# Optimization experiments

Hardware: AMD Instinct MI355X
Metric: run time of the kernel (lower is better)

The kernel has to match this reference:

```python
import jax, jax.numpy as jnp
import numpy as np

N_NODES = 100000
N_EDGES = 1600000
IN_FEATS = 128
HIDDEN = 128
N_CLASSES = 40
EPS = 1e-5  # BatchNorm1d default eps


def setup_inputs():
    key = jax.random.key(0)
    ks = jax.random.split(key, 12)
    s_in = 1.0 / np.sqrt(IN_FEATS)
    s_h = 1.0 / np.sqrt(HIDDEN)
    return {
        "feat": jax.random.normal(ks[0], (N_NODES, IN_FEATS), jnp.float32),
        "src": jax.random.randint(ks[1], (N_EDGES,), 0, N_NODES, jnp.int32),
        "dst": jax.random.randint(ks[2], (N_EDGES,), 0, N_NODES, jnp.int32),
        # GraphConv weights, stored (out, in) as in the torch module
        "w0": jax.random.normal(ks[3], (HIDDEN, IN_FEATS), jnp.float32) * s_in,
        "w1": jax.random.normal(ks[4], (HIDDEN, HIDDEN), jnp.float32) * s_h,
        "w2": jax.random.normal(ks[5], (N_CLASSES, HIDDEN), jnp.float32) * s_h,
        "b2": jnp.zeros((N_CLASSES,), jnp.float32),  # bias only on last layer
        # skip-connection linears (use_linear=True, bias=False)
        "l0": jax.random.normal(ks[6], (HIDDEN, IN_FEATS), jnp.float32) * s_in,
        "l1": jax.random.normal(ks[7], (HIDDEN, HIDDEN), jnp.float32) * s_h,
        "l2": jax.random.normal(ks[8], (N_CLASSES, HIDDEN), jnp.float32) * s_h,
        # BatchNorm affine params for the two hidden layers
        "g0": jnp.ones((HIDDEN,), jnp.float32),
        "beta0": jnp.zeros((HIDDEN,), jnp.float32),
        "g1": jnp.ones((HIDDEN,), jnp.float32),
        "beta1": jnp.zeros((HIDDEN,), jnp.float32),
    }


def _spmm(h, src, dst):
    # copy_u + sum aggregation: out[d] = sum_{e: dst[e]==d} h[src[e]]
    return jax.ops.segment_sum(h[src], dst, num_segments=N_NODES)


def gcn_forward(feat, src, dst, w0, w1, w2, b2, l0, l1, l2, g0, beta0, g1, beta1):
    ones = jnp.ones((src.shape[0],), jnp.float32)
    out_deg = jnp.clip(jax.ops.segment_sum(ones, src, num_segments=N_NODES), 1.0)
    in_deg = jnp.clip(jax.ops.segment_sum(ones, dst, num_segments=N_NODES), 1.0)
    out_norm = out_deg ** -0.5  # norm='both', applied to src features
    in_norm = in_deg ** -0.5    # norm='both', applied to aggregated result

    def conv(h, W, bias, in_gt_out):
        hs = h * out_norm[:, None]
        if in_gt_out:  # in_feats > out_feats: project first, then aggregate
            rst = _spmm(hs @ W.T, src, dst)
        else:          # aggregate first, then project
            rst = _spmm(hs, src, dst) @ W.T
        rst = rst * in_norm[:, None]
        if bias is not None:
            rst = rst + bias
        return rst

    def bn(x, g, b):
        mu = x.mean(0)
        var = x.var(0)  # biased variance, matches BN training-mode normalization
        return (x - mu) * jax.lax.rsqrt(var + EPS) * g + b

    h = feat  # dropout in eval mode = identity
    h = jax.nn.relu(bn(conv(h, w0, None, IN_FEATS > HIDDEN) + h @ l0.T, g0, beta0))
    h = jax.nn.relu(bn(conv(h, w1, None, False) + h @ l1.T, g1, beta1))
    h = conv(h, w2, b2, HIDDEN > N_CLASSES) + h @ l2.T
    return h


def reference(feat, src, dst, w0, w1, w2, b2, l0, l1, l2, g0, beta0, g1, beta1):
    return gcn_forward(feat, src, dst, w0, w1, w2, b2, l0, l1, l2, g0, beta0, g1, beta1)
```

## Files before the change

### kernel.cpp

```cpp
#include <hip/hip_runtime.h>
#include <hip/hip_fp16.h>
#include <cstdint>
#include <cstddef>

#define N_NODES 100000
#define N_EDGES 1600000
#define EPS 1e-5f

typedef _Float16 half8 __attribute__((ext_vector_type(8)));
typedef float floatx4 __attribute__((ext_vector_type(4)));

#define HCH 128
#define HRG 4
#define HBINS 32768
#define HWORDS (HBINS / 2)
#define HCHUNK (N_EDGES / HCH)
#define HCHUNK4 (HCHUNK / 4)

__global__ void k_hist_part(const int* __restrict__ keys, unsigned int* __restrict__ Hpart) {
  __shared__ unsigned int bins[HWORDS];
  int c = blockIdx.x % HCH, r = blockIdx.x / HCH;
  int base = r * HBINS;
  for (int i = threadIdx.x; i < HWORDS; i += 256) bins[i] = 0;
  __syncthreads();
  const int4* k4 = (const int4*)(keys + c * HCHUNK);
  for (int i = threadIdx.x; i < HCHUNK4; i += 256) {
    int4 k = k4[i];
    int a;
    a = k.x - base; if ((unsigned)a < (unsigned)HBINS) atomicAdd(&bins[a >> 1], 1u << ((a & 1) * 16));
    a = k.y - base; if ((unsigned)a < (unsigned)HBINS) atomicAdd(&bins[a >> 1], 1u << ((a & 1) * 16));
    a = k.z - base; if ((unsigned)a < (unsigned)HBINS) atomicAdd(&bins[a >> 1], 1u << ((a & 1) * 16));
    a = k.w - base; if ((unsigned)a < (unsigned)HBINS) atomicAdd(&bins[a >> 1], 1u << ((a & 1) * 16));
  }
  __syncthreads();
  unsigned int* outp = Hpart + ((size_t)blockIdx.x << 14);
  for (int i = threadIdx.x; i < HWORDS; i += 256) outp[i] = bins[i];
}

__global__ void k_hist_sum(const unsigned short* __restrict__ Hp, int* __restrict__ deg) {
  int b = blockIdx.x * 256 + threadIdx.x;
  if (b >= N_NODES) return;
  int r = b >> 15, lo = b & (HBINS - 1);
  const unsigned short* p = Hp + ((size_t)(r * HCH) << 15) + lo;
  unsigned int t = 0;
#pragma unroll 8
  for (int c = 0; c < HCH; ++c) t += p[(size_t)c << 15];
  deg[b] = (int)t;
}

__global__ void k_hist_scan(unsigned short* __restrict__ Hp, int* __restrict__ degd) {
  int b = blockIdx.x * 256 + threadIdx.x;
  if (b >= N_NODES) return;
  int r = b >> 15, lo = b & (HBINS - 1);
  unsigned short* p = Hp + ((size_t)(r * HCH) << 15) + lo;
  unsigned int t = 0;
#pragma unroll 8
  for (int c = 0; c < HCH; ++c) {
    unsigned int v = p[(size_t)c << 15];
    p[(size_t)c << 15] = (unsigned short)t;
    t += v;
  }
  degd[b] = (int)t;
}

__global__ void k_build(const int* __restrict__ src, const int* __restrict__ dst,
                        const unsigned short* __restrict__ Hbase,
                        const int* __restrict__ row_start, int* __restrict__ col) {
  __shared__ unsigned int cur[HWORDS];
  int c = blockIdx.x % HCH, r = blockIdx.x / HCH;
  int base = r * HBINS;
  for (int i = threadIdx.x; i < HWORDS; i += 256) cur[i] = 0;
  __syncthreads();
  const unsigned short* hb = Hbase + ((size_t)blockIdx.x << 15);
  const int4* d4 = (const int4*)(dst + c * HCHUNK);
  const int4* s4 = (const int4*)(src + c * HCHUNK);
  for (int i = threadIdx.x; i < HCHUNK4; i += 256) {
    int4 d = d4[i];
    int4 s = s4[i];
    int a;
    a = d.x - base;
    if ((unsigned)a < (unsigned)HBINS) {
      unsigned old = atomicAdd(&cur[a >> 1], 1u << ((a & 1) * 16));
      unsigned lr = (old >> ((a & 1) * 16)) & 0xffffu;
      col[row_start[d.x] + hb[a] + lr] = s.x;
    }
    a = d.y - base;
    if ((unsigned)a < (unsigned)HBINS) {
      unsigned old = atomicAdd(&cur[a >> 1], 1u << ((a & 1) * 16));
      unsigned lr = (old >> ((a & 1) * 16)) & 0xffffu;
      col[row_start[d.y] + hb[a] + lr] = s.y;
    }
    a = d.z - base;
    if ((unsigned)a < (unsigned)HBINS) {
      unsigned old = atomicAdd(&cur[a >> 1], 1u << ((a & 1) * 16));
      unsigned lr = (old >> ((a & 1) * 16)) & 0xffffu;
      col[row_start[d.z] + hb[a] + lr] = s.z;
    }
    a = d.w - base;
    if ((unsigned)a < (unsigned)HBINS) {
      unsigned old = atomicAdd(&cur[a >> 1], 1u << ((a & 1) * 16));
      unsigned lr = (old >> ((a & 1) * 16)) & 0xffffu;
      col[row_start[d.w] + hb[a] + lr] = s.w;
    }
  }
}

__global__ void k_norms(const int* __restrict__ degs, const int* __restrict__ degd,
                        float* out_norm, float* in_norm) {
  int i = blockIdx.x * 256 + threadIdx.x;
  if (i < N_NODES) {
    out_norm[i] = rsqrtf((float)max(degs[i], 1));
    in_norm[i]  = rsqrtf((float)max(degd[i], 1));
  }
}

__global__ void k_scan1(const int* __restrict__ degd, int* bsum) {
  __shared__ int s[256];
  int t = threadIdx.x;
  int i = blockIdx.x * 256 + t;
  s[t] = (i < N_NODES) ? degd[i] : 0;
  __syncthreads();
  for (int off = 128; off > 0; off >>= 1) {
    if (t < off) s[t] += s[t + off];
    __syncthreads();
  }
  if (t == 0) bsum[blockIdx.x] = s[0];
}

__global__ void k_scan2(int* bsum, int nb) {
  __shared__ int s[512];
  int t = threadIdx.x;
  int v = (t < nb) ? bsum[t] : 0;
  s[t] = v;
  __syncthreads();
  for (int off = 1; off < 512; off <<= 1) {
    int x = (t >= off) ? s[t - off] : 0;
    __syncthreads();
    s[t] += x;
    __syncthreads();
  }
  if (t < nb) bsum[t] = s[t] - v;
}

__global__ void k_scan3(const int* __restrict__ degd, const int* __restrict__ bsum,
                        int* row_start) {
  __shared__ int s[256];
  int t = threadIdx.x;
  int i = blockIdx.x * 256 + t;
  int v = (i < N_NODES) ? degd[i] : 0;
  s[t] = v;
  __syncthreads();
  for (int off = 1; off < 256; off <<= 1) {
    int x = (t >= off) ? s[t - off] : 0;
    __syncthreads();
    s[t] += x;
    __syncthreads();
  }
  if (i < N_NODES) row_start[i] = bsum[blockIdx.x] + s[t] - v;
  if (i == 0) row_start[N_NODES] = N_EDGES;
}

__global__ void k_w2h(const float* __restrict__ w0, const float* __restrict__ l0,
                      const float* __restrict__ w1, const float* __restrict__ l1,
                      const float* __restrict__ w2, const float* __restrict__ l2,
                      unsigned short* __restrict__ W) {
  int i = blockIdx.x * 256 + threadIdx.x;
  if (i >= 18944) return;
  int h = i * 4;
  const float* src; int off;
  if (h < 16384)      { src = w0; off = h; }
  else if (h < 32768) { src = l0; off = h - 16384; }
  else if (h < 49152) { src = w1; off = h - 32768; }
  else if (h < 65536) { src = l1; off = h - 49152; }
  else if (h < 70656) { src = w2; off = h - 65536; }
  else                { src = l2; off = h - 70656; }
  float4 v = *(const float4*)(src + off);
  ushort4 o;
  o.x = __half_as_ushort(__float2half_rn(v.x));
  o.y = __half_as_ushort(__float2half_rn(v.y));
  o.z = __half_as_ushort(__float2half_rn(v.z));
  o.w = __half_as_ushort(__float2half_rn(v.w));
  ((ushort4*)W)[i] = o;
}

__global__ void k_feat2h(const float* __restrict__ feat, const float* __restrict__ out_norm,
                         unsigned short* __restrict__ H, unsigned short* __restrict__ F) {
  int i = blockIdx.x * 256 + threadIdx.x;
  if (i >= N_NODES * 32) return;
  float on = out_norm[i >> 5];
  float4 v = ((const float4*)feat)[i];
  ushort4 s, u;
  s.x = __half_as_ushort(__float2half_rn(v.x * on));
  s.y = __half_as_ushort(__float2half_rn(v.y * on));
  s.z = __half_as_ushort(__float2half_rn(v.z * on));
  s.w = __half_as_ushort(__float2half_rn(v.w * on));
  u.x = __half_as_ushort(__float2half_rn(v.x));
  u.y = __half_as_ushort(__float2half_rn(v.y));
  u.z = __half_as_ushort(__float2half_rn(v.z));
  u.w = __half_as_ushort(__float2half_rn(v.w));
  ((ushort4*)H)[i] = s;
  ((ushort4*)F)[i] = u;
}

__global__ void k_agg128h(const __half* __restrict__ H, const int* __restrict__ col,
                          const int* __restrict__ row_start,
                          const float* __restrict__ in_norm,
                          unsigned short* __restrict__ out16) {
  int wave = threadIdx.x >> 6;
  int lane = threadIdx.x & 63;
  int node = blockIdx.x * 4 + wave;
  if (node >= N_NODES) return;
  int q = lane >> 4;
  int sub = lane & 15;
  int s0 = row_start[node], s1 = row_start[node + 1];
  const uint4* hp = (const uint4*)H;
  float a[8];
#pragma unroll
  for (int j = 0; j < 8; ++j) a[j] = 0.f;
  int e = s0 + q;
  for (; e + 4 < s1; e += 8) {
    int c0 = col[e];
    int c1 = col[e + 4];
    uint4 u0 = hp[(size_t)c0 * 16 + sub];
    uint4 u1 = hp[(size_t)c1 * 16 + sub];
    const __half2* h0 = (const __half2*)&u0;
    const __half2* h1 = (const __half2*)&u1;
#pragma unroll
    for (int j = 0; j < 4; ++j) {
      float2 f0 = __half22float2(h0[j]);
      float2 f1 = __half22float2(h1[j]);
      a[2 * j] += f0.x + f1.x;
      a[2 * j + 1] += f0.y + f1.y;
    }
  }
  if (e < s1) {
    uint4 u = hp[(size_t)col[e] * 16 + sub];
    const __half2* h0 = (const __half2*)&u;
#pragma unroll
    for (int j = 0; j < 4; ++j) {
      float2 f = __half22float2(h0[j]);
      a[2 * j] += f.x;
      a[2 * j + 1] += f.y;
    }
  }
#pragma unroll
  for (int j = 0; j < 8; ++j) {
    a[j] += __shfl_xor(a[j], 16);
    a[j] += __shfl_xor(a[j], 32);
  }
  if (q == 0) {
    float sc = in_norm[node];
    __half2 o[4];
#pragma unroll
    for (int j = 0; j < 4; ++j)
      o[j] = __float22half2_rn(make_float2(a[2 * j] * sc, a[2 * j + 1] * sc));
    ((uint4*)out16)[(size_t)node * 16 + sub] = *(const uint4*)o;
  }
}

__launch_bounds__(256)
__global__ void k_gemm_dual16(const unsigned short* __restrict__ Xa,
                              const unsigned short* __restrict__ Xh,
                              const unsigned short* __restrict__ W16,
                              unsigned short* __restrict__ Out16, float* __restrict__ pstats) {
  __shared__ __align__(16) unsigned short sX[64][136];
  __shared__ __align__(16) unsigned short sW[128][136];
  int t = threadIdx.x;
  int row0 = blockIdx.x * 64;
  int w = t >> 6, lane = t & 63;
  int q = lane >> 4, m = lane & 15;
  floatx4 acc[8];
#pragma unroll
  for (int i = 0; i < 8; ++i) acc[i] = (floatx4){0.f, 0.f, 0.f, 0.f};

  for (int phase = 0; phase < 2; ++phase) {
    const unsigned short* Xg = phase ? Xh : Xa;
    __syncthreads();
    {
#pragma unroll
      for (int it = 0; it < 4; ++it) {
        int idx = it * 256 + t;
        int r = idx >> 4, g = idx & 15;
        const uint4* xr = (const uint4*)(Xg + (size_t)min(row0 + r, N_NODES - 1) * 128);
        *(uint4*)&sX[r][g * 8] = xr[g];
      }
    }
    {
      const uint4* wsrc = (const uint4*)(W16 + ((size_t)phase << 14));
#pragma unroll
      for (int it = 0; it < 8; ++it) {
        int idx = it * 256 + t;
        int n = idx >> 4, g = idx & 15;
        *(uint4*)&sW[n][g * 8] = wsrc[idx];
      }
    }
    __syncthreads();
#pragma unroll
    for (int ks = 0; ks < 4; ++ks) {
      int kk = ks * 32 + q * 8;
      half8 a = *(const half8*)&sX[w * 16 + m][kk];
#pragma unroll
      for (int t8 = 0; t8 < 8; ++t8) {
        half8 b = *(const half8*)&sW[t8 * 16 + m][kk];
        acc[t8] = __builtin_amdgcn_mfma_f32_16x16x32_f16(a, b, acc[t8], 0, 0, 0);
      }
    }
  }
  float ps[8], pq[8];
#pragma unroll
  for (int t8 = 0; t8 < 8; ++t8) {
    int colj = t8 * 16 + m;
    float s = 0.f, sq = 0.f;
#pragma unroll
    for (int i = 0; i < 4; ++i) {
      int row = row0 + w * 16 + q * 4 + i;
      if (row < N_NODES) {
        float v = acc[t8][i];
        s += v; sq += v * v;
        Out16[(size_t)row * 128 + colj] = __half_as_ushort(__float2half_rn(v));
      }
    }
    s += __shfl_xor(s, 16);
    s += __shfl_xor(s, 32);
    sq += __shfl_xor(sq, 16);
    sq += __shfl_xor(sq, 32);
    ps[t8] = s; pq[t8] = sq;
  }
  __syncthreads();
  float* pSum = (float*)&sX[0][0];
  float* pSq = pSum + 512;
  if (q == 0) {
#pragma unroll
    for (int t8 = 0; t8 < 8; ++t8) {
      pSum[w * 128 + t8 * 16 + m] = ps[t8];
      pSq[w * 128 + t8 * 16 + m] = pq[t8];
    }
  }
  __syncthreads();
  if (t < 128) {
    float s = (pSum[t] + pSum[128 + t]) + (pSum[256 + t] + pSum[384 + t]);
    float sq = (pSq[t] + pSq[128 + t]) + (pSq[256 + t] + pSq[384 + t]);
    pstats[(size_t)blockIdx.x * 256 + t] = s;
    pstats[(size_t)blockIdx.x * 256 + 128 + t] = sq;
  }
}

__global__ void k_stats_red(const float* __restrict__ pstats, float* __restrict__ stats,
                            int nblk) {
  int t = threadIdx.x;
  float s = 0.f;
  for (int b = blockIdx.x; b < nblk; b += gridDim.x)
    s += pstats[(size_t)b * 256 + t];
  atomicAdd(&stats[t], s);
}

__global__ void k_bnrelu16(const unsigned short* __restrict__ x16,
                           const float* __restrict__ stats,
                           const float* __restrict__ g, const float* __restrict__ b,
                           const float* __restrict__ out_norm,
                           unsigned short* __restrict__ H, unsigned short* __restrict__ F) {
  int i = blockIdx.x * 256 + threadIdx.x;
  if (i >= N_NODES * 16) return;
  int c8 = (i & 15) * 8;
  uint4 raw = ((const uint4*)x16)[i];
  const __half2* hp2 = (const __half2*)&raw;
  float v[8];
#pragma unroll
  for (int j = 0; j < 4; ++j) {
    float2 f = __half22float2(hp2[j]);
    v[2 * j] = f.x;
    v[2 * j + 1] = f.y;
  }
  const float inv = 1.f / (float)N_NODES;
#pragma unroll
  for (int j = 0; j < 8; ++j) {
    int c = c8 + j;
    float mu = stats[c] * inv;
    float var = stats[128 + c] * inv - mu * mu;
    float rs = rsqrtf(var + EPS);
    float y = (v[j] - mu) * rs * g[c] + b[c];
    v[j] = y > 0.f ? y : 0.f;
  }
  if (H) {
    float on = out_norm[i >> 4];
    ushort4 o[2];
#pragma unroll
    for (int j = 0; j < 8; ++j) ((unsigned short*)o)[j] = __half_as_ushort(__float2half_rn(v[j] * on));
    ((uint4*)H)[i] = *(const uint4*)o;
  }
  if (F) {
    ushort4 o[2];
#pragma unroll
    for (int j = 0; j < 8; ++j) ((unsigned short*)o)[j] = __half_as_ushort(__float2half_rn(v[j]));
    ((uint4*)F)[i] = *(const uint4*)o;
  }
}

__launch_bounds__(256)
__global__ void k_gemm2_16(const unsigned short* __restrict__ X,
                           const unsigned short* __restrict__ W80,
                           const float* __restrict__ b2,
                           const float* __restrict__ out_norm,
                           __half* __restrict__ p, float* __restrict__ out) {
  __shared__ __align__(16) unsigned short sX[64][136];
  __shared__ __align__(16) unsigned short sW[80][136];
  int t = threadIdx.x;
  int row0 = blockIdx.x * 64;
  int w = t >> 6, lane = t & 63;
  int q = lane >> 4, m = lane & 15;
  {
#pragma unroll
    for (int it = 0; it < 4; ++it) {
      int idx = it * 256 + t;
      int r = idx >> 4, g = idx & 15;
      const uint4* xr = (const uint4*)(X + (size_t)min(row0 + r, N_NODES - 1) * 128);
      *(uint4*)&sX[r][g * 8] = xr[g];
    }
  }
  {
    const uint4* wsrc = (const uint4*)W80;
#pragma unroll
    for (int it = 0; it < 5; ++it) {
      int idx = it * 256 + t;
      int n = idx >> 4, g = idx & 15;
      *(uint4*)&sW[n][g * 8] = wsrc[idx];
    }
  }
  __syncthreads();
  floatx4 acc[5];
#pragma unroll
  for (int i = 0; i < 5; ++i) acc[i] = (floatx4){0.f, 0.f, 0.f, 0.f};
#pragma unroll
  for (int ks = 0; ks < 4; ++ks) {
    int kk = ks * 32 + q * 8;
    half8 a = *(const half8*)&sX[w * 16 + m][kk];
#pragma unroll
    for (int t5 = 0; t5 < 5; ++t5) {
      half8 b = *(const half8*)&sW[t5 * 16 + m][kk];
      acc[t5] = __builtin_amdgcn_mfma_f32_16x16x32_f16(a, b, acc[t5], 0, 0, 0);
    }
  }
#pragma unroll
  for (int t5 = 0; t5 < 5; ++t5) {
    int col = t5 * 16 + m;
#pragma unroll
    for (int i = 0; i < 4; ++i) {
      int row = row0 + w * 16 + q * 4 + i;
      if (row >= N_NODES) continue;
      if (col < 40) {
        p[(size_t)row * 64 + col] = __float2half_rn(out_norm[row] * acc[t5][i]);
      } else {
        out[(size_t)row * 40 + (col - 40)] = acc[t5][i] + b2[col - 40];
      }
    }
  }
  for (int idx = t; idx < 64 * 24; idx += 256) {
    int r = idx / 24, c = 40 + idx % 24;
    int row = row0 + r;
    if (row < N_NODES) p[(size_t)row * 64 + c] = __float2half_rn(0.f);
  }
}

__global__ void k_agg64h(const __half* __restrict__ p, const int* __restrict__ col,
                         const int* __restrict__ row_start,
                         const float* __restrict__ in_norm,
                         float* __restrict__ out) {
  int wave = threadIdx.x >> 6, lane = threadIdx.x & 63;
  int node = blockIdx.x * 4 + wave;
  if (node >= N_NODES) return;
  int oct = lane >> 3;
  int sub = lane & 7;
  int s0 = row_start[node], s1 = row_start[node + 1];
  const uint4* pp = (const uint4*)p;
  float a[8];
#pragma unroll
  for (int j = 0; j < 8; ++j) a[j] = 0.f;
  int e = s0 + oct;
  for (; e + 8 < s1; e += 16) {
    int c0 = col[e];
    int c1 = col[e + 8];
    uint4 u0 = pp[(size_t)c0 * 8 + sub];
    uint4 u1 = pp[(size_t)c1 * 8 + sub];
    const __half2* h0 = (const __half2*)&u0;
    const __half2* h1 = (const __half2*)&u1;
#pragma unroll
    for (int j = 0; j < 4; ++j) {
      float2 f0 = __half22float2(h0[j]);
      float2 f1 = __half22float2(h1[j]);
      a[2 * j] += f0.x + f1.x;
      a[2 * j + 1] += f0.y + f1.y;
    }
  }
  if (e < s1) {
    uint4 u = pp[(size_t)col[e] * 8 + sub];
    const __half2* h0 = (const __half2*)&u;
#pragma unroll
    for (int j = 0; j < 4; ++j) {
      float2 f = __half22float2(h0[j]);
      a[2 * j] += f.x;
      a[2 * j + 1] += f.y;
    }
  }
#pragma unroll
  for (int j = 0; j < 8; ++j) {
    a[j] += __shfl_xor(a[j], 8);
    a[j] += __shfl_xor(a[j], 16);
    a[j] += __shfl_xor(a[j], 32);
  }
  if (oct == 0 && sub < 5) {
    float sc = in_norm[node];
    float4* op = (float4*)(out + (size_t)node * 40 + (size_t)sub * 8);
    float4 v0 = op[0], v1 = op[1];
    v0.x += sc * a[0]; v0.y += sc * a[1]; v0.z += sc * a[2]; v0.w += sc * a[3];
    v1.x += sc * a[4]; v1.y += sc * a[5]; v1.z += sc * a[6]; v1.w += sc * a[7];
    op[0] = v0; op[1] = v1;
  }
}

extern "C" void kernel_launch(void* const* d_in, const int* in_sizes, int n_in,
                              void* d_out, int out_size, void* d_ws, size_t ws_size,
                              hipStream_t stream) {
  const float* feat = (const float*)d_in[0];
  const int* src = (const int*)d_in[1];
  const int* dst = (const int*)d_in[2];
  const float* w0 = (const float*)d_in[3];
  const float* w1 = (const float*)d_in[4];
  const float* w2 = (const float*)d_in[5];
  const float* b2 = (const float*)d_in[6];
  const float* l0 = (const float*)d_in[7];
  const float* l1 = (const float*)d_in[8];
  const float* l2 = (const float*)d_in[9];
  const float* g0 = (const float*)d_in[10];
  const float* beta0 = (const float*)d_in[11];
  const float* g1 = (const float*)d_in[12];
  const float* beta1 = (const float*)d_in[13];
  float* out = (float*)d_out;

  char* ws = (char*)d_ws;
  size_t off = 0;
  auto alloc = [&](size_t bytes) {
    void* ptr = ws + off;
    off = (off + bytes + 255) & ~(size_t)255;
    return ptr;
  };
  unsigned short* A16 = (unsigned short*)alloc(2 * (size_t)N_NODES * 128);
  float* B = (float*)alloc(sizeof(float) * (size_t)N_NODES * 128);
  unsigned short* H = (unsigned short*)alloc(2 * (size_t)N_NODES * 128);
  unsigned short* F = (unsigned short*)alloc(2 * (size_t)N_NODES * 128);
  int* degs = (int*)alloc(sizeof(int) * N_NODES);
  int* degd = (int*)alloc(sizeof(int) * N_NODES);
  int* row_start = (int*)alloc(sizeof(int) * (N_NODES + 1));
  int* colb = (int*)alloc(sizeof(int) * N_EDGES);
  float* out_norm = (float*)alloc(sizeof(float) * N_NODES);
  float* in_norm = (float*)alloc(sizeof(float) * N_NODES);
  int* bsum = (int*)alloc(sizeof(int) * 512);
  float* stats = (float*)alloc(sizeof(float) * 256);
  unsigned short* W16 = (unsigned short*)alloc(2 * (size_t)75776);
  int gb = (N_NODES + 63) / 64;
  float* pstats = (float*)alloc(sizeof(float) * (size_t)gb * 256);

  unsigned int* Hpart = (unsigned int*)B;
  unsigned short* B16 = (unsigned short*)B;

  int nb = (N_NODES + 255) / 256;
  int hb = HCH * HRG;

  k_w2h<<<74, 256, 0, stream>>>(w0, l0, w1, l1, w2, l2, W16);

  k_hist_part<<<hb, 256, 0, stream>>>(src, Hpart);
  k_hist_sum<<<nb, 256, 0, stream>>>((const unsigned short*)Hpart, degs);
  k_hist_part<<<hb, 256, 0, stream>>>(dst, Hpart);
  k_hist_scan<<<nb, 256, 0, stream>>>((unsigned short*)Hpart, degd);
  k_norms<<<nb, 256, 0, stream>>>(degs, degd, out_norm, in_norm);
  k_scan1<<<nb, 256, 0, stream>>>(degd, bsum);
  k_scan2<<<1, 512, 0, stream>>>(bsum, nb);
  k_scan3<<<nb, 256, 0, stream>>>(degd, bsum, row_start);
  k_build<<<hb, 256, 0, stream>>>(src, dst, (const unsigned short*)Hpart, row_start, colb);

  int ab = (N_NODES + 3) / 4;
  int fb = (N_NODES * 32 + 255) / 256;
  int hb16 = (N_NODES * 16 + 255) / 256;

  k_feat2h<<<fb, 256, 0, stream>>>(feat, out_norm, H, F);
  k_agg128h<<<ab, 256, 0, stream>>>((const __half*)H, colb, row_start, in_norm, A16);
  k_gemm_dual16<<<gb, 256, 0, stream>>>(A16, F, W16, B16, pstats);
  hipMemsetAsync(stats, 0, sizeof(float) * 256, stream);
  k_stats_red<<<32, 256, 0, stream>>>(pstats, stats, gb);
  k_bnrelu16<<<hb16, 256, 0, stream>>>(B16, stats, g0, beta0, out_norm, H, F);

  k_agg128h<<<ab, 256, 0, stream>>>((const __half*)H, colb, row_start, in_norm, A16);
  k_gemm_dual16<<<gb, 256, 0, stream>>>(A16, F, W16 + 32768, B16, pstats);
  hipMemsetAsync(stats, 0, sizeof(float) * 256, stream);
  k_stats_red<<<32, 256, 0, stream>>>(pstats, stats, gb);
  k_bnrelu16<<<hb16, 256, 0, stream>>>(B16, stats, g1, beta1, out_norm,
                                       (unsigned short*)nullptr, F);

  __half* p = (__half*)A16;
  k_gemm2_16<<<gb, 256, 0, stream>>>(F, W16 + 65536, b2, out_norm, p, out);
  k_agg64h<<<ab, 256, 0, stream>>>(p, colb, row_start, in_norm, out);
}
```

Measured before the change: 509.8 us.

## Replace histogram CSR build with global atomics and chunk-split aggregation

Swaps the partitioned shared-memory histogram and prefix-offset CSR build for direct global atomic degree counting and atomic cursor-based column placement. Splits 128-wide aggregation into 8 feature chunks, each handled by its own blocks and written in a chunk-major layout, so the gather of each chunk can stay cache-resident. The GEMM load is updated to read that chunked layout. Global atomics may contend, make the in-row edge order nondeterministic, and the chunked aggregation reissues the column-index reads for every chunk.

```diff
diff --git a/kernel.cpp b/kernel.cpp
--- a/kernel.cpp
+++ b/kernel.cpp
@@ -10,99 +10,16 @@
 typedef _Float16 half8 __attribute__((ext_vector_type(8)));
 typedef float floatx4 __attribute__((ext_vector_type(4)));
 
-#define HCH 128
-#define HRG 4
-#define HBINS 32768
-#define HWORDS (HBINS / 2)
-#define HCHUNK (N_EDGES / HCH)
-#define HCHUNK4 (HCHUNK / 4)
-
-__global__ void k_hist_part(const int* __restrict__ keys, unsigned int* __restrict__ Hpart) {
-  __shared__ unsigned int bins[HWORDS];
-  int c = blockIdx.x % HCH, r = blockIdx.x / HCH;
-  int base = r * HBINS;
-  for (int i = threadIdx.x; i < HWORDS; i += 256) bins[i] = 0;
-  __syncthreads();
-  const int4* k4 = (const int4*)(keys + c * HCHUNK);
-  for (int i = threadIdx.x; i < HCHUNK4; i += 256) {
-    int4 k = k4[i];
-    int a;
-    a = k.x - base; if ((unsigned)a < (unsigned)HBINS) atomicAdd(&bins[a >> 1], 1u << ((a & 1) * 16));
-    a = k.y - base; if ((unsigned)a < (unsigned)HBINS) atomicAdd(&bins[a >> 1], 1u << ((a & 1) * 16));
-    a = k.z - base; if ((unsigned)a < (unsigned)HBINS) atomicAdd(&bins[a >> 1], 1u << ((a & 1) * 16));
-    a = k.w - base; if ((unsigned)a < (unsigned)HBINS) atomicAdd(&bins[a >> 1], 1u << ((a & 1) * 16));
-  }
-  __syncthreads();
-  unsigned int* outp = Hpart + ((size_t)blockIdx.x << 14);
-  for (int i = threadIdx.x; i < HWORDS; i += 256) outp[i] = bins[i];
-}
-
-__global__ void k_hist_sum(const unsigned short* __restrict__ Hp, int* __restrict__ deg) {
-  int b = blockIdx.x * 256 + threadIdx.x;
-  if (b >= N_NODES) return;
-  int r = b >> 15, lo = b & (HBINS - 1);
-  const unsigned short* p = Hp + ((size_t)(r * HCH) << 15) + lo;
-  unsigned int t = 0;
-#pragma unroll 8
-  for (int c = 0; c < HCH; ++c) t += p[(size_t)c << 15];
-  deg[b] = (int)t;
-}
-
-__global__ void k_hist_scan(unsigned short* __restrict__ Hp, int* __restrict__ degd) {
-  int b = blockIdx.x * 256 + threadIdx.x;
-  if (b >= N_NODES) return;
-  int r = b >> 15, lo = b & (HBINS - 1);
-  unsigned short* p = Hp + ((size_t)(r * HCH) << 15) + lo;
-  unsigned int t = 0;
-#pragma unroll 8
-  for (int c = 0; c < HCH; ++c) {
-    unsigned int v = p[(size_t)c << 15];
-    p[(size_t)c << 15] = (unsigned short)t;
-    t += v;
-  }
-  degd[b] = (int)t;
-}
-
-__global__ void k_build(const int* __restrict__ src, const int* __restrict__ dst,
-                        const unsigned short* __restrict__ Hbase,
-                        const int* __restrict__ row_start, int* __restrict__ col) {
-  __shared__ unsigned int cur[HWORDS];
-  int c = blockIdx.x % HCH, r = blockIdx.x / HCH;
-  int base = r * HBINS;
-  for (int i = threadIdx.x; i < HWORDS; i += 256) cur[i] = 0;
-  __syncthreads();
-  const unsigned short* hb = Hbase + ((size_t)blockIdx.x << 15);
-  const int4* d4 = (const int4*)(dst + c * HCHUNK);
-  const int4* s4 = (const int4*)(src + c * HCHUNK);
-  for (int i = threadIdx.x; i < HCHUNK4; i += 256) {
-    int4 d = d4[i];
-    int4 s = s4[i];
-    int a;
-    a = d.x - base;
-    if ((unsigned)a < (unsigned)HBINS) {
-      unsigned old = atomicAdd(&cur[a >> 1], 1u << ((a & 1) * 16));
-      unsigned lr = (old >> ((a & 1) * 16)) & 0xffffu;
-      col[row_start[d.x] + hb[a] + lr] = s.x;
-    }
-    a = d.y - base;
-    if ((unsigned)a < (unsigned)HBINS) {
-      unsigned old = atomicAdd(&cur[a >> 1], 1u << ((a & 1) * 16));
-      unsigned lr = (old >> ((a & 1) * 16)) & 0xffffu;
-      col[row_start[d.y] + hb[a] + lr] = s.y;
-    }
-    a = d.z - base;
-    if ((unsigned)a < (unsigned)HBINS) {
-      unsigned old = atomicAdd(&cur[a >> 1], 1u << ((a & 1) * 16));
-      unsigned lr = (old >> ((a & 1) * 16)) & 0xffffu;
-      col[row_start[d.z] + hb[a] + lr] = s.z;
-    }
-    a = d.w - base;
-    if ((unsigned)a < (unsigned)HBINS) {
-      unsigned old = atomicAdd(&cur[a >> 1], 1u << ((a & 1) * 16));
-      unsigned lr = (old >> ((a & 1) * 16)) & 0xffffu;
-      col[row_start[d.w] + hb[a] + lr] = s.w;
-    }
-  }
+__global__ void k_deg(const int* __restrict__ src, const int* __restrict__ dst,
+                      int* __restrict__ degs, int* __restrict__ degd) {
+  int i = blockIdx.x * 256 + threadIdx.x;
+  if (i >= N_EDGES / 4) return;
+  int4 s = ((const int4*)src)[i];
+  int4 d = ((const int4*)dst)[i];
+  atomicAdd(&degs[s.x], 1); atomicAdd(&degs[s.y], 1);
+  atomicAdd(&degs[s.z], 1); atomicAdd(&degs[s.w], 1);
+  atomicAdd(&degd[d.x], 1); atomicAdd(&degd[d.y], 1);
+  atomicAdd(&degd[d.z], 1); atomicAdd(&degd[d.w], 1);
 }
 
 __global__ void k_norms(const int* __restrict__ degs, const int* __restrict__ degd,
@@ -158,6 +75,24 @@
   }
   if (i < N_NODES) row_start[i] = bsum[blockIdx.x] + s[t] - v;
   if (i == 0) row_start[N_NODES] = N_EDGES;
+}
+
+__global__ void k_initcur(const int* __restrict__ row_start, int* __restrict__ cur) {
+  int i = blockIdx.x * 256 + threadIdx.x;
+  if (i < N_NODES) cur[i] = row_start[i];
+}
+
+__global__ void k_build2(const int* __restrict__ src, const int* __restrict__ dst,
+                         int* __restrict__ cur, int* __restrict__ col) {
+  int i = blockIdx.x * 256 + threadIdx.x;
+  if (i >= N_EDGES / 4) return;
+  int4 s = ((const int4*)src)[i];
+  int4 d = ((const int4*)dst)[i];
+  int p;
+  p = atomicAdd(&cur[d.x], 1); col[p] = s.x;
+  p = atomicAdd(&cur[d.y], 1); col[p] = s.y;
+  p = atomicAdd(&cur[d.z], 1); col[p] = s.z;
+  p = atomicAdd(&cur[d.w], 1); col[p] = s.w;
 }
 
 __global__ void k_w2h(const float* __restrict__ w0, const float* __restrict__ l0,
@@ -202,59 +137,49 @@
   ((ushort4*)F)[i] = u;
 }
 
-__global__ void k_agg128h(const __half* __restrict__ H, const int* __restrict__ col,
-                          const int* __restrict__ row_start,
-                          const float* __restrict__ in_norm,
-                          unsigned short* __restrict__ out16) {
-  int wave = threadIdx.x >> 6;
-  int lane = threadIdx.x & 63;
-  int node = blockIdx.x * 4 + wave;
-  if (node >= N_NODES) return;
-  int q = lane >> 4;
-  int sub = lane & 15;
-  int s0 = row_start[node], s1 = row_start[node + 1];
+__global__ void k_aggc(const unsigned short* __restrict__ H, const int* __restrict__ col,
+                       const int* __restrict__ row_start, const float* __restrict__ in_norm,
+                       unsigned short* __restrict__ out16c) {
+  int chunk = blockIdx.x & 7;
+  int grp = blockIdx.x >> 3;
+  int t = threadIdx.x;
+  int lane = t & 63;
+  int wv = t >> 6;
+  int node = grp * 128 + wv * 32 + (lane >> 1);
+  int sub = lane & 1;
+  bool valid = node < N_NODES;
+  int s0 = 0, s1 = 0;
+  if (valid) { s0 = row_start[node]; s1 = row_start[node + 1]; }
   const uint4* hp = (const uint4*)H;
+  size_t coff = (size_t)chunk * 2 + sub;
   float a[8];
 #pragma unroll
   for (int j = 0; j < 8; ++j) a[j] = 0.f;
-  int e = s0 + q;
-  for (; e + 4 < s1; e += 8) {
-    int c0 = col[e];
-    int c1 = col[e + 4];
-    uint4 u0 = hp[(size_t)c0 * 16 + sub];
-    uint4 u1 = hp[(size_t)c1 * 16 + sub];
-    const __half2* h0 = (const __half2*)&u0;
-    const __half2* h1 = (const __half2*)&u1;
-#pragma unroll
-    for (int j = 0; j < 4; ++j) {
-      float2 f0 = __half22float2(h0[j]);
-      float2 f1 = __half22float2(h1[j]);
-      a[2 * j] += f0.x + f1.x;
-      a[2 * j + 1] += f0.y + f1.y;
-    }
-  }
-  if (e < s1) {
-    uint4 u = hp[(size_t)col[e] * 16 + sub];
-    const __half2* h0 = (const __half2*)&u;
-#pragma unroll
-    for (int j = 0; j < 4; ++j) {
-      float2 f = __half22float2(h0[j]);
-      a[2 * j] += f.x;
-      a[2 * j + 1] += f.y;
-    }
-  }
-#pragma unroll
-  for (int j = 0; j < 8; ++j) {
-    a[j] += __shfl_xor(a[j], 16);
-    a[j] += __shfl_xor(a[j], 32);
-  }
-  if (q == 0) {
+  int e = s0;
+  while (__any(e < s1)) {
+#pragma unroll
+    for (int k = 0; k < 4; ++k) {
+      if (e + k < s1) {
+        int c = col[e + k];
+        uint4 u = hp[(size_t)c * 16 + coff];
+        const __half2* h2p = (const __half2*)&u;
+#pragma unroll
+        for (int j = 0; j < 4; ++j) {
+          float2 f = __half22float2(h2p[j]);
+          a[2 * j] += f.x;
+          a[2 * j + 1] += f.y;
+        }
+      }
+    }
+    e += 4;
+  }
+  if (valid) {
     float sc = in_norm[node];
     __half2 o[4];
 #pragma unroll
     for (int j = 0; j < 4; ++j)
       o[j] = __float22half2_rn(make_float2(a[2 * j] * sc, a[2 * j + 1] * sc));
-    ((uint4*)out16)[(size_t)node * 16 + sub] = *(const uint4*)o;
+    ((uint4*)out16c)[((size_t)chunk * N_NODES + node) * 2 + sub] = *(const uint4*)o;
   }
 }
 
@@ -274,14 +199,24 @@
   for (int i = 0; i < 8; ++i) acc[i] = (floatx4){0.f, 0.f, 0.f, 0.f};
 
   for (int phase = 0; phase < 2; ++phase) {
-    const unsigned short* Xg = phase ? Xh : Xa;
-    __syncthreads();
-    {
+    __syncthreads();
+    if (phase == 0) {
+      const uint4* xc = (const uint4*)Xa;
+#pragma unroll
+      for (int it = 0; it < 4; ++it) {
+        int idx = it * 256 + t;
+        int p = idx >> 7;
+        int n = (idx >> 1) & 63;
+        int sb = idx & 1;
+        int row = min(row0 + n, N_NODES - 1);
+        *(uint4*)&sX[n][p * 16 + sb * 8] = xc[((size_t)p * N_NODES + row) * 2 + sb];
+      }
+    } else {
 #pragma unroll
       for (int it = 0; it < 4; ++it) {
         int idx = it * 256 + t;
         int r = idx >> 4, g = idx & 15;
-        const uint4* xr = (const uint4*)(Xg + (size_t)min(row0 + r, N_NODES - 1) * 128);
+        const uint4* xr = (const uint4*)(Xh + (size_t)min(row0 + r, N_NODES - 1) * 128);
         *(uint4*)&sX[r][g * 8] = xr[g];
       }
     }
@@ -558,37 +493,38 @@
   unsigned short* W16 = (unsigned short*)alloc(2 * (size_t)75776);
   int gb = (N_NODES + 63) / 64;
   float* pstats = (float*)alloc(sizeof(float) * (size_t)gb * 256);
-
-  unsigned int* Hpart = (unsigned int*)B;
+  int* cursor = (int*)alloc(sizeof(int) * N_NODES);
+
   unsigned short* B16 = (unsigned short*)B;
 
   int nb = (N_NODES + 255) / 256;
-  int hb = HCH * HRG;
+  int eb4 = (N_EDGES / 4 + 255) / 256;
 
   k_w2h<<<74, 256, 0, stream>>>(w0, l0, w1, l1, w2, l2, W16);
 
-  k_hist_part<<<hb, 256, 0, stream>>>(src, Hpart);
-  k_hist_sum<<<nb, 256, 0, stream>>>((const unsigned short*)Hpart, degs);
-  k_hist_part<<<hb, 256, 0, stream>>>(dst, Hpart);
-  k_hist_scan<<<nb, 256, 0, stream>>>((unsigned short*)Hpart, degd);
+  hipMemsetAsync(degs, 0, sizeof(int) * N_NODES, stream);
+  hipMemsetAsync(degd, 0, sizeof(int) * N_NODES, stream);
+  k_deg<<<eb4, 256, 0, stream>>>(src, dst, degs, degd);
   k_norms<<<nb, 256, 0, stream>>>(degs, degd, out_norm, in_norm);
   k_scan1<<<nb, 256, 0, stream>>>(degd, bsum);
   k_scan2<<<1, 512, 0, stream>>>(bsum, nb);
   k_scan3<<<nb, 256, 0, stream>>>(degd, bsum, row_start);
-  k_build<<<hb, 256, 0, stream>>>(src, dst, (const unsigned short*)Hpart, row_start, colb);
+  k_initcur<<<nb, 256, 0, stream>>>(row_start, cursor);
+  k_build2<<<eb4, 256, 0, stream>>>(src, dst, cursor, colb);
 
   int ab = (N_NODES + 3) / 4;
+  int cb = 8 * ((N_NODES + 127) / 128);
   int fb = (N_NODES * 32 + 255) / 256;
   int hb16 = (N_NODES * 16 + 255) / 256;
 
   k_feat2h<<<fb, 256, 0, stream>>>(feat, out_norm, H, F);
-  k_agg128h<<<ab, 256, 0, stream>>>((const __half*)H, colb, row_start, in_norm, A16);
+  k_aggc<<<cb, 256, 0, stream>>>(H, colb, row_start, in_norm, A16);
   k_gemm_dual16<<<gb, 256, 0, stream>>>(A16, F, W16, B16, pstats);
   hipMemsetAsync(stats, 0, sizeof(float) * 256, stream);
   k_stats_red<<<32, 256, 0, stream>>>(pstats, stats, gb);
   k_bnrelu16<<<hb16, 256, 0, stream>>>(B16, stats, g0, beta0, out_norm, H, F);
 
-  k_agg128h<<<ab, 256, 0, stream>>>((const __half*)H, colb, row_start, in_norm, A16);
+  k_aggc<<<cb, 256, 0, stream>>>(H, colb, row_start, in_norm, A16);
   k_gemm_dual16<<<gb, 256, 0, stream>>>(A16, F, W16 + 32768, B16, pstats);
   hipMemsetAsync(stats, 0, sizeof(float) * 256, stream);
   k_stats_red<<<32, 256, 0, stream>>>(pstats, stats, gb);
```

After: 1.073 ms. 2.11x slower.
